# Kernel tuning notes

Hardware: AMD Instinct MI355X
Metric: run time of the kernel (lower is better)

Reference implementation:

```python
import jax, jax.numpy as jnp
import numpy as np

EPS = 1e-5


def _extract3x3(x, stride=1):
    # channel-major patch extraction: output [B, C*9, Ho, Wo], each channel's 3x3 window contiguous
    B, C, H, W = x.shape
    xp = jnp.pad(x, ((0, 0), (0, 0), (1, 1), (1, 1)))
    Ho = (H + 2 - 3) // stride + 1
    Wo = (W + 2 - 3) // stride + 1
    pats = [xp[:, :, i:i + (Ho - 1) * stride + 1:stride, j:j + (Wo - 1) * stride + 1:stride]
            for i in range(3) for j in range(3)]
    return jnp.stack(pats, axis=2).reshape(B, C * 9, Ho, Wo)


def _amm(patches, centroids, lut, inv_temp):
    # patches: [B, D, H, W] channel-major, D = ncodebooks * subvec_len
    # centroids: [ncb, k, sub], lut: [ncb, k, out_channels]
    B, D, H, W = patches.shape
    ncb, k, sub = centroids.shape
    v = patches.reshape(B, ncb, sub, H * W).transpose(0, 3, 1, 2)  # [B, L, ncb, sub]
    # negative squared distance to each codeword (||v||^2 dropped: constant over k)
    scores = 2.0 * jnp.einsum('blcs,cks->blck', v, centroids) - jnp.sum(centroids * centroids, -1)[None, None]
    attn = jax.nn.softmax(scores * inv_temp, axis=-1)          # soft codeword assignment
    out = jnp.einsum('blck,cko->blo', attn, lut)                # LUT gather/sum over codebooks
    return out.transpose(0, 2, 1).reshape(B, -1, H, W)


def _bn(x, g, b):
    m = x.mean((0, 2, 3), keepdims=True)
    v = x.var((0, 2, 3), keepdims=True)
    return g[None, :, None, None] * (x - m) * jax.lax.rsqrt(v + EPS) + b[None, :, None, None]


def setup_inputs() -> dict:
    key = jax.random.key(0)
    ks = jax.random.split(key, 8)
    B, C, H, W = 32, 1024, 14, 14
    width, out_c, K = 256, 1024, 16
    return {
        'x': jax.random.normal(ks[0], (B, C, H, W), jnp.float32),
        'c1_centroids': jax.random.normal(ks[1], (C // 4, K, 4), jnp.float32),
        'c1_lut': jax.random.normal(ks[2], (C // 4, K, width), jnp.float32) * 0.05,
        'c1_invt': jnp.ones((), jnp.float32),
        'c2_centroids': jax.random.normal(ks[3], (width, K, 9), jnp.float32),
        'c2_lut': jax.random.normal(ks[4], (width, K, width), jnp.float32) * 0.05,
        'c2_invt': jnp.ones((), jnp.float32),
        'c3_centroids': jax.random.normal(ks[5], (width // 4, K, 4), jnp.float32),
        'c3_lut': jax.random.normal(ks[6], (width // 4, K, out_c), jnp.float32) * 0.05,
        'c3_invt': jnp.ones((), jnp.float32),
        'bn1_g': jnp.ones((width,), jnp.float32), 'bn1_b': jnp.zeros((width,), jnp.float32),
        'bn2_g': jnp.ones((width,), jnp.float32), 'bn2_b': jnp.zeros((width,), jnp.float32),
        'bn3_g': jnp.ones((out_c,), jnp.float32), 'bn3_b': jnp.zeros((out_c,), jnp.float32),
    }


def reference(x, c1_centroids, c1_lut, c1_invt, c2_centroids, c2_lut, c2_invt,
              c3_centroids, c3_lut, c3_invt, bn1_g, bn1_b, bn2_g, bn2_b, bn3_g, bn3_b):
    identity = x
    out = _amm(x, c1_centroids, c1_lut, c1_invt)                 # amm_conv1x1, stride 1
    out = jax.nn.relu(_bn(out, bn1_g, bn1_b))
    out = _amm(_extract3x3(out, 1), c2_centroids, c2_lut, c2_invt)  # amm_conv3x3, stride 1, pad 1
    out = jax.nn.relu(_bn(out, bn2_g, bn2_b))
    out = _amm(out, c3_centroids, c3_lut, c3_invt)               # amm_conv1x1
    out = _bn(out, bn3_g, bn3_b)
    return jax.nn.relu(out + identity)
```

## Files before the change

kernel.cpp:

```cpp
#include <hip/hip_runtime.h>
#include <hip/hip_bf16.h>

#define EPSV 1e-5f

typedef unsigned short u16;
typedef __attribute__((ext_vector_type(8))) short short8;
typedef __attribute__((ext_vector_type(4))) float f32x4;
typedef __hip_bfloat16 bf16;

__device__ __forceinline__ unsigned int pack2(float a, float b) {
  bf16 ha = __float2bfloat16(a), hb = __float2bfloat16(b);
  u16 ua, ub;
  __builtin_memcpy(&ua, &ha, 2);
  __builtin_memcpy(&ub, &hb, 2);
  return (unsigned int)ua | ((unsigned int)ub << 16);
}

typedef __attribute__((address_space(1))) const void gvoid_t;
typedef __attribute__((address_space(3))) void lvoid_t;
__device__ __forceinline__ void gload16(const void* g, void* l) {
  __builtin_amdgcn_global_load_lds((gvoid_t*)g, (lvoid_t*)l, 16, 0, 0);
}


__global__ __launch_bounds__(256) void prep_kernel(
    const float* __restrict__ x, const float* __restrict__ cent,
    const float* __restrict__ invt, u16* __restrict__ attn,
    const float* __restrict__ s1, bf16* __restrict__ d1,
    const float* __restrict__ s2, bf16* __restrict__ d2,
    const float* __restrict__ s3, bf16* __restrict__ d3)
{
  __shared__ __align__(16) float sh[7012];
  const int tid = threadIdx.x;
  if (blockIdx.x >= 1024) {
    const int bid = blockIdx.x - 1024;
    const int which = bid >> 8, sub = bid & 255;
    const float* in = (which == 0) ? s1 : (which == 1) ? s2 : s3;
    bf16* out = (which == 0) ? d1 : (which == 1) ? d2 : d3;
    const int K = (which == 2) ? 1024 : 4096;
    const int N = (which == 2) ? 1024 : 256;
    const int kt = K >> 6;
    const int bk = sub & (kt - 1), bn = sub / kt;
    const int k0 = bk * 64, n0 = bn * 64;
    float* t = sh;
    for (int idx = tid; idx < 4096; idx += 256) {
      int r = idx >> 6, c = idx & 63;
      t[r * 65 + c] = in[(size_t)(k0 + r) * N + n0 + c];
    }
    __syncthreads();
    for (int idx = tid; idx < 4096; idx += 256) {
      int r = idx >> 6, c = idx & 63;
      out[(size_t)(n0 + r) * K + k0 + c] = __float2bfloat16(t[c * 65 + r]);
    }
    return;
  }
  float* vs = sh;
  float* cs = sh + 6468;
  const int bi = blockIdx.x >> 5, cg = blockIdx.x & 31;
  const float* xb = x + ((size_t)bi * 1024 + cg * 32) * 196;
  for (int e = tid; e < 3136; e += 256) {
    int c = e / 98, p2 = e - c * 98;
    float2 w = *(const float2*)&xb[(size_t)c * 196 + p2 * 2];
    vs[(p2 * 2) * 33 + c] = w.x;
    vs[(p2 * 2 + 1) * 33 + c] = w.y;
  }
  if (tid < 128) {
    int cb = tid >> 4, kk = tid & 15;
    *(float4*)&cs[cb * 68 + kk * 4] =
        *(const float4*)&cent[(size_t)(cg * 8 + cb) * 64 + kk * 4];
  }
  __syncthreads();
  const float it = invt[0];
  const int cbL = tid & 7, pj = tid >> 3;
  float4 cv[16]; float cn[16];
  #pragma unroll
  for (int k = 0; k < 16; k++) {
    cv[k] = *(const float4*)&cs[cbL * 68 + k * 4];
    cn[k] = cv[k].x * cv[k].x + cv[k].y * cv[k].y + cv[k].z * cv[k].z + cv[k].w * cv[k].w;
  }
  for (int p = pj; p < 196; p += 32) {
    const float* vp = &vs[p * 33 + cbL * 4];
    const float v0 = vp[0], v1 = vp[1], v2 = vp[2], v3 = vp[3];
    float s[16], mx = -3e38f;
    #pragma unroll
    for (int k = 0; k < 16; k++) {
      float d = v0 * cv[k].x + v1 * cv[k].y + v2 * cv[k].z + v3 * cv[k].w;
      s[k] = it * (2.f * d - cn[k]);
      mx = fmaxf(mx, s[k]);
    }
    float sum = 0.f;
    #pragma unroll
    for (int k = 0; k < 16; k++) { float e = __expf(s[k] - mx); s[k] = e; sum += e; }
    const float r = 1.f / sum;
    uint4 w0, w1;
    w0.x = pack2(s[0] * r,  s[1] * r);  w0.y = pack2(s[2] * r,  s[3] * r);
    w0.z = pack2(s[4] * r,  s[5] * r);  w0.w = pack2(s[6] * r,  s[7] * r);
    w1.x = pack2(s[8] * r,  s[9] * r);  w1.y = pack2(s[10] * r, s[11] * r);
    w1.z = pack2(s[12] * r, s[13] * r); w1.w = pack2(s[14] * r, s[15] * r);
    uint4* dst = (uint4*)(attn + (size_t)(bi * 196 + p) * 4096 + (cg * 8 + cbL) * 16);
    dst[0] = w0; dst[1] = w1;
  }
}

__global__ __launch_bounds__(256) void attn2_kernel(const float* __restrict__ out1,
    const float* __restrict__ g, const float* __restrict__ bb,
    const float* __restrict__ Sacc, const float* __restrict__ cent,
    const float* __restrict__ invt, u16* __restrict__ attn)
{
  __shared__ float vs[4 * 16 * 16];
  __shared__ __align__(16) float cs[16 * 196];
  __shared__ float cnl[16 * 17];
  __shared__ float ssl[32];
  const int tid = threadIdx.x;
  const int rp = blockIdx.x >> 4, cg = blockIdx.x & 15;
  const int b = rp / 7, y0 = (rp % 7) * 2, m0 = rp * 28;
  const float it = invt[0];
  if (tid < 16) {
    const int ch = cg * 16 + tid;
    float S = Sacc[ch], S2 = Sacc[256 + ch];
    float mean = S * (1.f / 6272.f);
    float var = S2 * (1.f / 6272.f) - mean * mean;
    float sc = g[ch] * rsqrtf(var + EPSV);
    ssl[tid] = sc; ssl[16 + tid] = bb[ch] - mean * sc;
  }
  __syncthreads();
  for (int e = tid; e < 1024; e += 256) {
    int c = e & 15, x1 = (e >> 4) & 15, dyy = e >> 8;
    int yy = y0 + dyy - 1, xx = x1 - 1;
    float v = 0.f;
    int ch = cg * 16 + c;
    if (yy >= 0 && yy < 14 && xx >= 0 && xx < 14) {
      float val = out1[(size_t)((b * 14 + yy) * 14 + xx) * 256 + ch];
      v = fmaxf(val * ssl[c] + ssl[16 + c], 0.f);
    }
    vs[e] = v;
  }
  const float it2 = 2.f * it;
  for (int idx = tid; idx < 576; idx += 256) {
    int cb = idx / 36, f4i = idx - cb * 36;
    float4 w = *(const float4*)&cent[(size_t)(cg * 16 + cb) * 144 + f4i * 4];
    int j0 = f4i * 4;
    #pragma unroll
    for (int t = 0; t < 4; t++) {
      int j = j0 + t, k = j / 9, jj = j - k * 9;
      cs[cb * 196 + k * 12 + jj] = it2 * ((const float*)&w)[t];
    }
  }
  if (tid < 256) {
    int cb = tid >> 4, k = tid & 15;
    const float* cc = &cent[(size_t)(cg * 16 + cb) * 144 + k * 9];
    float cn = 0.f;
    #pragma unroll
    for (int j = 0; j < 9; j++) cn = fmaf(cc[j], cc[j], cn);
    cnl[cb * 17 + k] = it * cn;
  }
  __syncthreads();
  const int cb = tid & 15, pq = tid >> 4;
  const int np = (pq < 12) ? 2 : 1;
  float v[2][9];
  #pragma unroll
  for (int i = 0; i < 2; i++) if (i < np) {
    const int p = i * 16 + pq;
    const int r = p / 14, xc = p - r * 14;
    #pragma unroll
    for (int dy = 0; dy < 3; dy++)
      #pragma unroll
      for (int dx = 0; dx < 3; dx++)
        v[i][dy * 3 + dx] = vs[((r + dy) * 16 + xc + dx) * 16 + cb];
  }
  float s[2][16];
  #pragma unroll
  for (int k = 0; k < 16; k++) {
    const float* ck = &cs[cb * 196 + k * 12];
    const float4 ca = *(const float4*)ck;
    const float4 cbv = *(const float4*)(ck + 4);
    const float c8 = ck[8];
    const float cnv = cnl[cb * 17 + k];
    float c9[9] = {ca.x, ca.y, ca.z, ca.w, cbv.x, cbv.y, cbv.z, cbv.w, c8};
    #pragma unroll
    for (int i = 0; i < 2; i++) if (i < np) {
      float d = -cnv;
      #pragma unroll
      for (int j = 0; j < 9; j++) d = fmaf(c9[j], v[i][j], d);
      s[i][k] = d;
    }
  }
  #pragma unroll
  for (int i = 0; i < 2; i++) if (i < np) {
    float mx = -3e38f;
    #pragma unroll
    for (int k = 0; k < 16; k++) mx = fmaxf(mx, s[i][k]);
    float sum = 0.f;
    #pragma unroll
    for (int k = 0; k < 16; k++) { float e = __expf(s[i][k] - mx); s[i][k] = e; sum += e; }
    const float r = 1.f / sum;
    const int p = i * 16 + pq;
    uint4 w0, w1;
    w0.x = pack2(s[i][0] * r,  s[i][1] * r);  w0.y = pack2(s[i][2] * r,  s[i][3] * r);
    w0.z = pack2(s[i][4] * r,  s[i][5] * r);  w0.w = pack2(s[i][6] * r,  s[i][7] * r);
    w1.x = pack2(s[i][8] * r,  s[i][9] * r);  w1.y = pack2(s[i][10] * r, s[i][11] * r);
    w1.z = pack2(s[i][12] * r, s[i][13] * r); w1.w = pack2(s[i][14] * r, s[i][15] * r);
    uint4* dst = (uint4*)(attn + (size_t)(m0 + p) * 4096 + (cg * 16 + cb) * 16);
    dst[0] = w0; dst[1] = w1;
  }
}

__global__ __launch_bounds__(256) void attn3_kernel(const float* __restrict__ out2,
    const float* __restrict__ g, const float* __restrict__ bb,
    const float* __restrict__ Sacc, const float* __restrict__ cent,
    const float* __restrict__ invt, bf16* __restrict__ attn)
{
  __shared__ float ssl[512];
  const int t = threadIdx.x;
  {
    float S = Sacc[t], S2 = Sacc[256 + t];
    float mean = S * (1.f / 6272.f);
    float var = S2 * (1.f / 6272.f) - mean * mean;
    float sc = g[t] * rsqrtf(var + EPSV);
    ssl[t] = sc; ssl[256 + t] = bb[t] - mean * sc;
  }
  __syncthreads();
  const int cb = t & 63, ml = t >> 6;
  const int m0 = blockIdx.x * 16;
  const float it = invt[0];
  float4 cv[16]; float cn[16];
  const float4* cc = (const float4*)(cent + cb * 64);
  #pragma unroll
  for (int k = 0; k < 16; k++) {
    cv[k] = cc[k];
    cn[k] = cv[k].x * cv[k].x + cv[k].y * cv[k].y + cv[k].z * cv[k].z + cv[k].w * cv[k].w;
  }
  const float4 scv = *(const float4*)(ssl + cb * 4);
  const float4 shv = *(const float4*)(ssl + 256 + cb * 4);
  for (int gi = 0; gi < 4; gi++) {
    const int m = m0 + gi * 4 + ml;
    float4 xv = *(const float4*)(out2 + (size_t)m * 256 + cb * 4);
    float4 v;
    v.x = fmaxf(xv.x * scv.x + shv.x, 0.f);
    v.y = fmaxf(xv.y * scv.y + shv.y, 0.f);
    v.z = fmaxf(xv.z * scv.z + shv.z, 0.f);
    v.w = fmaxf(xv.w * scv.w + shv.w, 0.f);
    float s[16], mx = -3e38f;
    #pragma unroll
    for (int k = 0; k < 16; k++) {
      float d = v.x * cv[k].x + v.y * cv[k].y + v.z * cv[k].z + v.w * cv[k].w;
      s[k] = it * (2.f * d - cn[k]);
      mx = fmaxf(mx, s[k]);
    }
    float sum = 0.f;
    #pragma unroll
    for (int k = 0; k < 16; k++) { float e = __expf(s[k] - mx); s[k] = e; sum += e; }
    float r = 1.f / sum;
    #pragma unroll
    for (int k = 0; k < 16; k++)
      attn[(size_t)m * 1024 + cb * 16 + k] = __float2bfloat16(s[k] * r);
  }
}

template<int KDIM, int NT, int KSLICES, int BM, int BK>
__global__ __launch_bounds__(512) void gemm_kernel(const u16* __restrict__ A,
    const u16* __restrict__ Bt, float* __restrict__ C, size_t cstride,
    float* __restrict__ zacc, int zn, float* __restrict__ stats)
{
  constexpr int NDIM = NT * 128;
  constexpr int KS = KDIM / KSLICES;
  constexpr int MT = 6272 / BM;
  constexpr int FM = BM / 64;
  constexpr int KU = BK / 32;
  constexpr int SLOTS = BK / 8;
  constexpr int RPC = 64 / SLOTS;
  constexpr int ACALLS = BM / (RPC * 8);
  constexpr int BCALLS = 128 / (RPC * 8);
  __shared__ __align__(16) u16 Asm[2][BM * BK];
  __shared__ __align__(16) u16 Bsm[2][128 * BK];
  const int tid = threadIdx.x;
  if (blockIdx.x == 0 && zacc) {
    for (int i = tid; i < zn; i += 512) zacc[i] = 0.f;
  }
  const int nwg = gridDim.x;
  int wg = blockIdx.x;
  if ((nwg & 7) == 0) wg = (blockIdx.x & 7) * (nwg >> 3) + (blockIdx.x >> 3);
  const int nt = wg % NT;
  const int mt = (wg / NT) % MT;
  const int sl = wg / (NT * MT);
  const int kbeg = sl * KS, kend = kbeg + KS;
  const int m0 = mt * BM, n0 = nt * 128;
  const int lane = tid & 63, wid = tid >> 6;
  const int wm = wid >> 1, wn = wid & 1;
  const int lr = lane / SLOTS, sslot = lane % SLOTS;
  const int gs = sslot ^ (lr & 7);

  f32x4 acc[FM][4];
  #pragma unroll
  for (int i = 0; i < FM; i++)
    #pragma unroll
    for (int j = 0; j < 4; j++) acc[i][j] = (f32x4){0.f, 0.f, 0.f, 0.f};

  const u16* Abase = A + (size_t)m0 * KDIM;
  const u16* Bbase = Bt + (size_t)n0 * KDIM;

  auto stage = [&](int bf, int kb) {
    #pragma unroll
    for (int c = 0; c < ACALLS; c++) {
      const int r0 = (wid * ACALLS + c) * RPC;
      gload16(Abase + (size_t)(r0 + lr) * KDIM + kb + gs * 8, &Asm[bf][r0 * BK]);
    }
    #pragma unroll
    for (int c = 0; c < BCALLS; c++) {
      const int r0 = (wid * BCALLS + c) * RPC;
      gload16(Bbase + (size_t)(r0 + lr) * KDIM + kb + gs * 8, &Bsm[bf][r0 * BK]);
    }
  };

  auto compute = [&](int bf) {
    #pragma unroll
    for (int ks = 0; ks < KU; ks++) {
      short8 a[FM], b[4];
      #pragma unroll
      for (int f = 0; f < FM; f++) {
        const int ra = wm * (BM / 4) + f * 16 + (lane & 15);
        const int ja = (ks * 4 + (lane >> 4)) ^ (ra & 7);
        a[f] = *(const short8*)(&Asm[bf][ra * BK + ja * 8]);
      }
      #pragma unroll
      for (int f = 0; f < 4; f++) {
        const int rb = wn * 64 + f * 16 + (lane & 15);
        const int jb = (ks * 4 + (lane >> 4)) ^ (rb & 7);
        b[f] = *(const short8*)(&Bsm[bf][rb * BK + jb * 8]);
      }
      #pragma unroll
      for (int fm = 0; fm < FM; fm++)
        #pragma unroll
        for (int fn = 0; fn < 4; fn++)
          acc[fm][fn] = __builtin_amdgcn_mfma_f32_16x16x32_bf16(a[fm], b[fn], acc[fm][fn], 0, 0, 0);
    }
  };

  stage(0, kbeg);
  __syncthreads();
  int cur = 0;
  for (int kb = kbeg + BK; kb < kend; kb += BK) {
    stage(cur ^ 1, kb);
    compute(cur);
    __syncthreads();
    cur ^= 1;
  }
  compute(cur);

  float* __restrict__ Cs = C + (size_t)sl * cstride;
  #pragma unroll
  for (int fm = 0; fm < FM; fm++)
    #pragma unroll
    for (int fn = 0; fn < 4; fn++) {
      const int col = n0 + wn * 64 + fn * 16 + (lane & 15);
      const int rbase = m0 + wm * (BM / 4) + fm * 16 + (lane >> 4) * 4;
      #pragma unroll
      for (int r = 0; r < 4; r++)
        Cs[(size_t)(rbase + r) * NDIM + col] = acc[fm][fn][r];
    }

  if (stats) {
    __syncthreads();
    float* red = (float*)&Asm[0][0];
    #pragma unroll
    for (int fn = 0; fn < 4; fn++) {
      float s = 0.f, s2 = 0.f;
      #pragma unroll
      for (int fm = 0; fm < FM; fm++)
        #pragma unroll
        for (int r = 0; r < 4; r++) {
          float v = acc[fm][fn][r];
          s += v; s2 = fmaf(v, v, s2);
        }
      s += __shfl_xor(s, 16);  s += __shfl_xor(s, 32);
      s2 += __shfl_xor(s2, 16); s2 += __shfl_xor(s2, 32);
      if ((lane >> 4) == 0) {
        const int colL = wn * 64 + fn * 16 + (lane & 15);
        red[wm * 256 + colL] = s;
        red[wm * 256 + 128 + colL] = s2;
      }
    }
    __syncthreads();
    if (tid < 256) {
      const int colL = tid & 127, st = (tid >> 7) & 1;
      float v = red[st * 128 + colL] + red[256 + st * 128 + colL]
              + red[512 + st * 128 + colL] + red[768 + st * 128 + colL];
      atomicAdd(&stats[(size_t)st * NDIM + n0 + colL], v);
    }
  }
}

template<int CH, int NBLK, int NSUM>
__global__ __launch_bounds__(256) void bnpart_kernel(const float* __restrict__ buf,
    float* __restrict__ sum_out, float* __restrict__ acc)
{
  constexpr int PC = CH / 256;
  constexpr int ROWS = 6272 / NBLK;
  constexpr size_t PSTR = 6272ull * CH;
  const int t = threadIdx.x, m0 = blockIdx.x * ROWS;
  float s[PC], s2[PC];
  #pragma unroll
  for (int j = 0; j < PC; j++) { s[j] = 0.f; s2[j] = 0.f; }
  for (int i = 0; i < ROWS; i++) {
    const size_t ro = (size_t)(m0 + i) * CH;
    #pragma unroll
    for (int j = 0; j < PC; j++) {
      float v = buf[ro + t + j * 256];
      #pragma unroll
      for (int n = 1; n < NSUM; n++) v += buf[(size_t)n * PSTR + ro + t + j * 256];
      if (NSUM > 1) sum_out[ro + t + j * 256] = v;
      s[j] += v; s2[j] = fmaf(v, v, s2[j]);
    }
  }
  #pragma unroll
  for (int j = 0; j < PC; j++) {
    atomicAdd(&acc[t + j * 256], s[j]);
    atomicAdd(&acc[CH + t + j * 256], s2[j]);
  }
}

__global__ __launch_bounds__(256) void tfinal_kernel(const float* __restrict__ out3,
    const float* __restrict__ g, const float* __restrict__ bb,
    const float* __restrict__ Sacc, const float* __restrict__ x,
    float* __restrict__ out)
{
  __shared__ float t[64 * 199];
  __shared__ float ssl[128];
  const int b = blockIdx.x >> 4, n0 = (blockIdx.x & 15) * 64;
  if (threadIdx.x < 64) {
    const int ch = n0 + threadIdx.x;
    float S = Sacc[ch], S2 = Sacc[1024 + ch];
    float mean = S * (1.f / 6272.f);
    float var = S2 * (1.f / 6272.f) - mean * mean;
    float sc = g[ch] * rsqrtf(var + EPSV);
    ssl[threadIdx.x] = sc; ssl[64 + threadIdx.x] = bb[ch] - mean * sc;
  }
  __syncthreads();
  for (int idx = threadIdx.x; idx < 196 * 64; idx += 256) {
    int p = idx >> 6, ni = idx & 63;
    float v = out3[(size_t)(b * 196 + p) * 1024 + n0 + ni] * ssl[ni] + ssl[64 + ni];
    t[ni * 199 + p] = v;
  }
  __syncthreads();
  for (int idx = threadIdx.x; idx < 64 * 196; idx += 256) {
    int ni = idx / 196, p = idx - ni * 196;
    size_t o = (size_t)(b * 1024 + n0 + ni) * 196 + p;
    out[o] = fmaxf(t[ni * 199 + p] + x[o], 0.f);
  }
}


template<int CIN, int OUT, bool APPLY_BN>
__global__ __launch_bounds__(256) void amm1x1_kernel(
    const float* __restrict__ xin, const float* __restrict__ ss,
    const float* __restrict__ cent, const float* __restrict__ lut,
    const float* __restrict__ invt, float* __restrict__ outbuf)
{
  constexpr int NCB = CIN / 4;
  constexpr int NO = OUT / 256;
  __shared__ float vsm[CIN * 14];
  __shared__ __align__(16) float attn_sm[14 * 16];
  const int tid = threadIdx.x;
  const int b = blockIdx.x / 14, y = blockIdx.x % 14;
  const int rowbase = y * 14;
  for (int e = tid; e < CIN * 14; e += 256) {
    int c = e / 14, xc = e - c * 14;
    float v = xin[(b * CIN + c) * 196 + rowbase + xc];
    if (APPLY_BN) v = fmaxf(v * ss[c] + ss[CIN + c], 0.f);
    vsm[e] = v;
  }
  __syncthreads();
  float acc[14 * NO];
  #pragma unroll
  for (int i = 0; i < 14 * NO; i++) acc[i] = 0.f;
  const float it = invt[0];
  const int p_ = tid >> 4, k_ = tid & 15;
  for (int cb = 0; cb < NCB; ++cb) {
    if (tid < 224) {
      const float* cc = cent + (cb * 16 + k_) * 4;
      float s = 0.f;
      #pragma unroll
      for (int si = 0; si < 4; si++) {
        float cv = cc[si];
        float vv = vsm[(cb * 4 + si) * 14 + p_];
        s = fmaf(cv, 2.f * vv - cv, s);
      }
      s *= it;
      float m = s;
      #pragma unroll
      for (int off = 8; off; off >>= 1) m = fmaxf(m, __shfl_xor(m, off, 16));
      float e = __expf(s - m);
      float sum = e;
      #pragma unroll
      for (int off = 8; off; off >>= 1) sum += __shfl_xor(sum, off, 16);
      attn_sm[p_ * 16 + k_] = e / sum;
    }
    __syncthreads();
    float lv[NO][16];
    #pragma unroll
    for (int j = 0; j < NO; j++)
      #pragma unroll
      for (int k = 0; k < 16; k++)
        lv[j][k] = lut[(cb * 16 + k) * OUT + j * 256 + tid];
    const float4* a4 = (const float4*)attn_sm;
    #pragma unroll
    for (int p = 0; p < 14; p++) {
      float4 q0 = a4[p*4+0], q1 = a4[p*4+1], q2 = a4[p*4+2], q3 = a4[p*4+3];
      float av[16] = {q0.x,q0.y,q0.z,q0.w, q1.x,q1.y,q1.z,q1.w,
                      q2.x,q2.y,q2.z,q2.w, q3.x,q3.y,q3.z,q3.w};
      #pragma unroll
      for (int j = 0; j < NO; j++) {
        float s = acc[p * NO + j];
        #pragma unroll
        for (int k = 0; k < 16; k++) s = fmaf(av[k], lv[j][k], s);
        acc[p * NO + j] = s;
      }
    }
    __syncthreads();
  }
  #pragma unroll
  for (int j = 0; j < NO; j++) {
    int o = j * 256 + tid;
    #pragma unroll
    for (int p = 0; p < 14; p++)
      outbuf[(b * OUT + o) * 196 + rowbase + p] = acc[p * NO + j];
  }
}

__global__ __launch_bounds__(256) void amm3x3_kernel(
    const float* __restrict__ xin, const float* __restrict__ ss,
    const float* __restrict__ cent, const float* __restrict__ lut,
    const float* __restrict__ invt, float* __restrict__ outbuf)
{
  __shared__ float vsm[256 * 3 * 16];
  __shared__ __align__(16) float attn_sm[14 * 16];
  const int tid = threadIdx.x;
  const int b = blockIdx.x / 14, y = blockIdx.x % 14;
  for (int e = tid; e < 256 * 3 * 16; e += 256) {
    int c = e / 48, rem = e - c * 48, i = rem >> 4, col = rem & 15;
    int yy = y + i - 1, xx = col - 1;
    float v = 0.f;
    if (yy >= 0 && yy < 14 && xx >= 0 && xx < 14) {
      v = xin[(b * 256 + c) * 196 + yy * 14 + xx];
      v = fmaxf(v * ss[c] + ss[256 + c], 0.f);
    }
    vsm[e] = v;
  }
  __syncthreads();
  float acc[14];
  #pragma unroll
  for (int i = 0; i < 14; i++) acc[i] = 0.f;
  const float it = invt[0];
  const int p_ = tid >> 4, k_ = tid & 15;
  for (int cb = 0; cb < 256; ++cb) {
    if (tid < 224) {
      const float* cc = cent + (cb * 16 + k_) * 9;
      float s = 0.f;
      #pragma unroll
      for (int i = 0; i < 3; i++)
        #pragma unroll
        for (int j = 0; j < 3; j++) {
          float cv = cc[i * 3 + j];
          float vv = vsm[(cb * 3 + i) * 16 + p_ + j];
          s = fmaf(cv, 2.f * vv - cv, s);
        }
      s *= it;
      float m = s;
      #pragma unroll
      for (int off = 8; off; off >>= 1) m = fmaxf(m, __shfl_xor(m, off, 16));
      float e = __expf(s - m);
      float sum = e;
      #pragma unroll
      for (int off = 8; off; off >>= 1) sum += __shfl_xor(sum, off, 16);
      attn_sm[p_ * 16 + k_] = e / sum;
    }
    __syncthreads();
    float lv[16];
    #pragma unroll
    for (int k = 0; k < 16; k++) lv[k] = lut[(cb * 16 + k) * 256 + tid];
    const float4* a4 = (const float4*)attn_sm;
    #pragma unroll
    for (int p = 0; p < 14; p++) {
      float4 q0 = a4[p*4+0], q1 = a4[p*4+1], q2 = a4[p*4+2], q3 = a4[p*4+3];
      float av[16] = {q0.x,q0.y,q0.z,q0.w, q1.x,q1.y,q1.z,q1.w,
                      q2.x,q2.y,q2.z,q2.w, q3.x,q3.y,q3.z,q3.w};
      float s = acc[p];
      #pragma unroll
      for (int k = 0; k < 16; k++) s = fmaf(av[k], lv[k], s);
      acc[p] = s;
    }
    __syncthreads();
  }
  #pragma unroll
  for (int p = 0; p < 14; p++)
    outbuf[(b * 256 + tid) * 196 + y * 14 + p] = acc[p];
}

template<int CH>
__global__ __launch_bounds__(256) void bnstats_kernel(const float* __restrict__ buf,
    const float* __restrict__ g, const float* __restrict__ bb, float* __restrict__ ss)
{
  const int c = blockIdx.x, tid = threadIdx.x;
  float s = 0.f, s2 = 0.f;
  for (int e = tid; e < 32 * 196; e += 256) {
    int bi = e / 196, l = e - bi * 196;
    float v = buf[(bi * CH + c) * 196 + l];
    s += v; s2 = fmaf(v, v, s2);
  }
  #pragma unroll
  for (int off = 32; off; off >>= 1) { s += __shfl_down(s, off); s2 += __shfl_down(s2, off); }
  __shared__ float red[8];
  int w = tid >> 6;
  if ((tid & 63) == 0) { red[w] = s; red[4 + w] = s2; }
  __syncthreads();
  if (tid == 0) {
    float S  = red[0] + red[1] + red[2] + red[3];
    float S2 = red[4] + red[5] + red[6] + red[7];
    float mean = S * (1.f / 6272.f);
    float var  = S2 * (1.f / 6272.f) - mean * mean;
    float sc = g[c] * rsqrtf(var + EPSV);
    ss[c] = sc;
    ss[CH + c] = bb[c] - mean * sc;
  }
}

__global__ __launch_bounds__(256) void final_old_kernel(float* __restrict__ out3,
    const float* __restrict__ ss, const float* __restrict__ x)
{
  const int total = 32 * 1024 * 196;
  for (int idx = blockIdx.x * 256 + threadIdx.x; idx < total; idx += gridDim.x * 256) {
    int c = (idx / 196) & 1023;
    float v = out3[idx] * ss[c] + ss[1024 + c] + x[idx];
    out3[idx] = fmaxf(v, 0.f);
  }
}


extern "C" void kernel_launch(void* const* d_in, const int* in_sizes, int n_in,
                              void* d_out, int out_size, void* d_ws, size_t ws_size,
                              hipStream_t stream) {
  const float* x   = (const float*)d_in[0];
  const float* c1c = (const float*)d_in[1];
  const float* c1l = (const float*)d_in[2];
  const float* c1t = (const float*)d_in[3];
  const float* c2c = (const float*)d_in[4];
  const float* c2l = (const float*)d_in[5];
  const float* c2t = (const float*)d_in[6];
  const float* c3c = (const float*)d_in[7];
  const float* c3l = (const float*)d_in[8];
  const float* c3t = (const float*)d_in[9];
  const float* g1  = (const float*)d_in[10];
  const float* b1  = (const float*)d_in[11];
  const float* g2  = (const float*)d_in[12];
  const float* b2  = (const float*)d_in[13];
  const float* g3  = (const float*)d_in[14];
  const float* b3  = (const float*)d_in[15];

  float* ws = (float*)d_ws;
  const size_t FAST_NEED = 24255488ull * 4ull;

  if (ws_size >= FAST_NEED) {
    u16*   attnB = (u16*)ws;
    float* partC = ws + 12845056;
    float* out1  = partC + 6422528;
    float* out2  = out1 + 1605632;
    bf16*  lutT1 = (bf16*)(out2 + 1605632);
    bf16*  lutT2 = lutT1 + 1048576;
    bf16*  lutT3 = lutT2 + 1048576;
    float* acc1  = (float*)(lutT3 + 1048576);
    float* acc2  = acc1 + 512;
    float* acc3  = acc2 + 512;
    float* out3  = partC;
    const size_t PART_STRIDE = 1605632;

    prep_kernel<<<1792, 256, 0, stream>>>(x, c1c, c1t, attnB,
                                          c1l, lutT1, c2l, lutT2, c3l, lutT3);

    gemm_kernel<4096, 2, 4, 128, 64><<<392, 512, 0, stream>>>(
        attnB, (const u16*)lutT1, partC, PART_STRIDE, acc1, 512, nullptr);
    bnpart_kernel<256, 196, 4><<<196, 256, 0, stream>>>(partC, out1, acc1);

    attn2_kernel<<<3584, 256, 0, stream>>>(out1, g1, b1, acc1, c2c, c2t, attnB);
    gemm_kernel<4096, 2, 4, 128, 64><<<392, 512, 0, stream>>>(
        attnB, (const u16*)lutT2, partC, PART_STRIDE, acc2, 2560, nullptr);
    bnpart_kernel<256, 196, 4><<<196, 256, 0, stream>>>(partC, out2, acc2);

    attn3_kernel<<<392, 256, 0, stream>>>(out2, g2, b2, acc2, c3c, c3t, (bf16*)attnB);
    gemm_kernel<1024, 8, 1, 128, 64><<<392, 512, 0, stream>>>(
        attnB, (const u16*)lutT3, out3, 0, nullptr, 0, acc3);

    tfinal_kernel<<<512, 256, 0, stream>>>(out3, g3, b3, acc3, x, (float*)d_out);
  } else {
    float* out3 = (float*)d_out;
    float* out1 = ws;
    float* out2 = out1 + 32 * 256 * 196;
    float* ss1  = out2 + 32 * 256 * 196;
    float* ss2  = ss1 + 512;
    float* ss3  = ss2 + 512;

    amm1x1_kernel<1024, 256, false><<<448, 256, 0, stream>>>(x, nullptr, c1c, c1l, c1t, out1);
    bnstats_kernel<256><<<256, 256, 0, stream>>>(out1, g1, b1, ss1);
    amm3x3_kernel<<<448, 256, 0, stream>>>(out1, ss1, c2c, c2l, c2t, out2);
    bnstats_kernel<256><<<256, 256, 0, stream>>>(out2, g2, b2, ss2);
    amm1x1_kernel<256, 1024, true><<<448, 256, 0, stream>>>(out2, ss2, c3c, c3l, c3t, out3);
    bnstats_kernel<1024><<<1024, 256, 0, stream>>>(out3, g3, b3, ss3);
    final_old_kernel<<<2048, 256, 0, stream>>>(out3, ss3, x);
  }
}
```

Before: 275.2 us.

## Process a whole image per block in attn2 to amortize centroid setup and halo loads

attn2_kernel now gives each block a full 14x14 image for one 16-channel group, instead of a two-row strip. The block cuts from 3584 to 512. The centroid and norm tables are staged into shared memory once per image, and the input tile is loaded with vectorized float4 reads without redundant halo rows. Each thread then loops over positions in pairs. This removes repeated per-block setup and halo reloading, at the cost of fewer blocks (less parallelism) and a larger shared-memory footprint.

```diff
diff --git a/kernel.cpp b/kernel.cpp
--- a/kernel.cpp
+++ b/kernel.cpp
@@ -107,13 +107,12 @@
     const float* __restrict__ Sacc, const float* __restrict__ cent,
     const float* __restrict__ invt, u16* __restrict__ attn)
 {
-  __shared__ float vs[4 * 16 * 16];
+  __shared__ float vs[16 * 16 * 16];
   __shared__ __align__(16) float cs[16 * 196];
   __shared__ float cnl[16 * 17];
   __shared__ float ssl[32];
   const int tid = threadIdx.x;
-  const int rp = blockIdx.x >> 4, cg = blockIdx.x & 15;
-  const int b = rp / 7, y0 = (rp % 7) * 2, m0 = rp * 28;
+  const int bi = blockIdx.x >> 4, cg = blockIdx.x & 15;
   const float it = invt[0];
   if (tid < 16) {
     const int ch = cg * 16 + tid;
@@ -123,18 +122,7 @@
     float sc = g[ch] * rsqrtf(var + EPSV);
     ssl[tid] = sc; ssl[16 + tid] = bb[ch] - mean * sc;
   }
-  __syncthreads();
-  for (int e = tid; e < 1024; e += 256) {
-    int c = e & 15, x1 = (e >> 4) & 15, dyy = e >> 8;
-    int yy = y0 + dyy - 1, xx = x1 - 1;
-    float v = 0.f;
-    int ch = cg * 16 + c;
-    if (yy >= 0 && yy < 14 && xx >= 0 && xx < 14) {
-      float val = out1[(size_t)((b * 14 + yy) * 14 + xx) * 256 + ch];
-      v = fmaxf(val * ssl[c] + ssl[16 + c], 0.f);
-    }
-    vs[e] = v;
-  }
+  for (int e = tid; e < 4096; e += 256) vs[e] = 0.f;
   const float it2 = 2.f * it;
   for (int idx = tid; idx < 576; idx += 256) {
     int cb = idx / 36, f4i = idx - cb * 36;
@@ -146,7 +134,7 @@
       cs[cb * 196 + k * 12 + jj] = it2 * ((const float*)&w)[t];
     }
   }
-  if (tid < 256) {
+  {
     int cb = tid >> 4, k = tid & 15;
     const float* cc = &cent[(size_t)(cg * 16 + cb) * 144 + k * 9];
     float cn = 0.f;
@@ -155,53 +143,69 @@
     cnl[cb * 17 + k] = it * cn;
   }
   __syncthreads();
-  const int cb = tid & 15, pq = tid >> 4;
-  const int np = (pq < 12) ? 2 : 1;
-  float v[2][9];
-  #pragma unroll
-  for (int i = 0; i < 2; i++) if (i < np) {
-    const int p = i * 16 + pq;
-    const int r = p / 14, xc = p - r * 14;
-    #pragma unroll
-    for (int dy = 0; dy < 3; dy++)
-      #pragma unroll
-      for (int dx = 0; dx < 3; dx++)
-        v[i][dy * 3 + dx] = vs[((r + dy) * 16 + xc + dx) * 16 + cb];
-  }
-  float s[2][16];
-  #pragma unroll
-  for (int k = 0; k < 16; k++) {
-    const float* ck = &cs[cb * 196 + k * 12];
-    const float4 ca = *(const float4*)ck;
-    const float4 cbv = *(const float4*)(ck + 4);
-    const float c8 = ck[8];
-    const float cnv = cnl[cb * 17 + k];
-    float c9[9] = {ca.x, ca.y, ca.z, ca.w, cbv.x, cbv.y, cbv.z, cbv.w, c8};
+  for (int e = tid; e < 784; e += 256) {
+    int p = e >> 2, c4 = e & 3;
+    int r = p / 14, xc = p - r * 14;
+    float4 w = *(const float4*)&out1[(size_t)(bi * 196 + p) * 256 + cg * 16 + c4 * 4];
+    float* dst = &vs[((r + 1) * 16 + (xc + 1)) * 16 + c4 * 4];
+    dst[0] = fmaxf(w.x * ssl[c4 * 4 + 0] + ssl[16 + c4 * 4 + 0], 0.f);
+    dst[1] = fmaxf(w.y * ssl[c4 * 4 + 1] + ssl[16 + c4 * 4 + 1], 0.f);
+    dst[2] = fmaxf(w.z * ssl[c4 * 4 + 2] + ssl[16 + c4 * 4 + 2], 0.f);
+    dst[3] = fmaxf(w.w * ssl[c4 * 4 + 3] + ssl[16 + c4 * 4 + 3], 0.f);
+  }
+  __syncthreads();
+  const int cb = tid & 15, pj = tid >> 4;
+  for (int i0 = 0; i0 < 13; i0 += 2) {
+    const int p0 = pj + (i0 << 4);
+    const int p1 = pj + ((i0 + 1) << 4);
+    const int np = (p1 < 196) ? 2 : ((p0 < 196) ? 1 : 0);
+    if (np == 0) break;
+    float v[2][9];
     #pragma unroll
     for (int i = 0; i < 2; i++) if (i < np) {
-      float d = -cnv;
-      #pragma unroll
-      for (int j = 0; j < 9; j++) d = fmaf(c9[j], v[i][j], d);
-      s[i][k] = d;
-    }
-  }
-  #pragma unroll
-  for (int i = 0; i < 2; i++) if (i < np) {
-    float mx = -3e38f;
-    #pragma unroll
-    for (int k = 0; k < 16; k++) mx = fmaxf(mx, s[i][k]);
-    float sum = 0.f;
-    #pragma unroll
-    for (int k = 0; k < 16; k++) { float e = __expf(s[i][k] - mx); s[i][k] = e; sum += e; }
-    const float r = 1.f / sum;
-    const int p = i * 16 + pq;
-    uint4 w0, w1;
-    w0.x = pack2(s[i][0] * r,  s[i][1] * r);  w0.y = pack2(s[i][2] * r,  s[i][3] * r);
-    w0.z = pack2(s[i][4] * r,  s[i][5] * r);  w0.w = pack2(s[i][6] * r,  s[i][7] * r);
-    w1.x = pack2(s[i][8] * r,  s[i][9] * r);  w1.y = pack2(s[i][10] * r, s[i][11] * r);
-    w1.z = pack2(s[i][12] * r, s[i][13] * r); w1.w = pack2(s[i][14] * r, s[i][15] * r);
-    uint4* dst = (uint4*)(attn + (size_t)(m0 + p) * 4096 + (cg * 16 + cb) * 16);
-    dst[0] = w0; dst[1] = w1;
+      const int p = i ? p1 : p0;
+      const int r = p / 14, xc = p - r * 14;
+      #pragma unroll
+      for (int dy = 0; dy < 3; dy++)
+        #pragma unroll
+        for (int dx = 0; dx < 3; dx++)
+          v[i][dy * 3 + dx] = vs[((r + dy) * 16 + xc + dx) * 16 + cb];
+    }
+    float s[2][16];
+    #pragma unroll
+    for (int k = 0; k < 16; k++) {
+      const float* ck = &cs[cb * 196 + k * 12];
+      const float4 ca = *(const float4*)ck;
+      const float4 cbv = *(const float4*)(ck + 4);
+      const float c8 = ck[8];
+      const float cnv = cnl[cb * 17 + k];
+      float c9[9] = {ca.x, ca.y, ca.z, ca.w, cbv.x, cbv.y, cbv.z, cbv.w, c8};
+      #pragma unroll
+      for (int i = 0; i < 2; i++) if (i < np) {
+        float d = -cnv;
+        #pragma unroll
+        for (int j = 0; j < 9; j++) d = fmaf(c9[j], v[i][j], d);
+        s[i][k] = d;
+      }
+    }
+    #pragma unroll
+    for (int i = 0; i < 2; i++) if (i < np) {
+      const int p = i ? p1 : p0;
+      float mx = -3e38f;
+      #pragma unroll
+      for (int k = 0; k < 16; k++) mx = fmaxf(mx, s[i][k]);
+      float sum = 0.f;
+      #pragma unroll
+      for (int k = 0; k < 16; k++) { float e = __expf(s[i][k] - mx); s[i][k] = e; sum += e; }
+      const float r = 1.f / sum;
+      uint4 w0, w1;
+      w0.x = pack2(s[i][0] * r,  s[i][1] * r);  w0.y = pack2(s[i][2] * r,  s[i][3] * r);
+      w0.z = pack2(s[i][4] * r,  s[i][5] * r);  w0.w = pack2(s[i][6] * r,  s[i][7] * r);
+      w1.x = pack2(s[i][8] * r,  s[i][9] * r);  w1.y = pack2(s[i][10] * r, s[i][11] * r);
+      w1.z = pack2(s[i][12] * r, s[i][13] * r); w1.w = pack2(s[i][14] * r, s[i][15] * r);
+      uint4* dst = (uint4*)(attn + (size_t)(bi * 196 + p) * 4096 + (cg * 16 + cb) * 16);
+      dst[0] = w0; dst[1] = w1;
+    }
   }
 }
 
@@ -680,7 +684,7 @@
         attnB, (const u16*)lutT1, partC, PART_STRIDE, acc1, 512, nullptr);
     bnpart_kernel<256, 196, 4><<<196, 256, 0, stream>>>(partC, out1, acc1);
 
-    attn2_kernel<<<3584, 256, 0, stream>>>(out1, g1, b1, acc1, c2c, c2t, attnB);
+    attn2_kernel<<<512, 256, 0, stream>>>(out1, g1, b1, acc1, c2c, c2t, attnB);
     gemm_kernel<4096, 2, 4, 128, 64><<<392, 512, 0, stream>>>(
         attnB, (const u16*)lutT2, partC, PART_STRIDE, acc2, 2560, nullptr);
     bnpart_kernel<256, 196, 4><<<196, 256, 0, stream>>>(partC, out2, acc2);
```

New measurement: 264.0 us. -4.1%, faster.
